# Kernel optimization log

Measured on AMD Instinct MI355X. Metric: run time of the kernel, lower is better.

## Reference

```python
import jax, jax.numpy as jnp
import numpy as np

N = 50000      # nodes
E = 800000     # edges
F_IN = 256
H1, D1 = 4, 32   # conv1 heads, per-head dim (hidden_features)
H2, D2 = 1, 32   # conv2 heads, per-head dim (out_features)
NEG_SLOPE = 0.2


def setup_inputs():
    key = jax.random.key(0)
    ks = jax.random.split(key, 12)
    x = jax.random.normal(ks[0], (N, F_IN), dtype=jnp.float32)
    src = jax.random.randint(ks[1], (E,), 0, N, dtype=jnp.int32)
    dst = jax.random.randint(ks[2], (E,), 0, N, dtype=jnp.int32)
    s = 0.05
    W1 = jax.random.normal(ks[3], (F_IN, H1 * D1), dtype=jnp.float32) * s
    al1 = jax.random.normal(ks[4], (H1, D1), dtype=jnp.float32) * s
    ar1 = jax.random.normal(ks[5], (H1, D1), dtype=jnp.float32) * s
    b1 = jnp.zeros((H1 * D1,), dtype=jnp.float32)
    W2 = jax.random.normal(ks[6], (H1 * D1, H2 * D2), dtype=jnp.float32) * s
    al2 = jax.random.normal(ks[7], (H2, D2), dtype=jnp.float32) * s
    ar2 = jax.random.normal(ks[8], (H2, D2), dtype=jnp.float32) * s
    b2 = jnp.zeros((H2 * D2,), dtype=jnp.float32)
    return {"x": x, "W1": W1, "al1": al1, "ar1": ar1, "b1": b1,
            "W2": W2, "al2": al2, "ar2": ar2, "b2": b2,
            "src": src, "dst": dst}


def gat_layer(x, W, al, ar, b, src, dst, H, D):
    # x: [N, F] -> feat: [N, H, D]
    feat = (x @ W).reshape(-1, H, D)
    el = jnp.sum(feat * al, axis=-1)   # [N, H]
    er = jnp.sum(feat * ar, axis=-1)   # [N, H]
    # per-edge attention logits, LeakyReLU
    e = jax.nn.leaky_relu(el[src] + er[dst], negative_slope=NEG_SLOPE)  # [E, H]
    # edge softmax over destination neighborhoods (stable)
    m = jax.ops.segment_max(e, dst, num_segments=N)          # [N, H]
    m = jnp.where(jnp.isfinite(m), m, 0.0)                   # guard zero-in-degree
    ee = jnp.exp(e - m[dst])                                 # [E, H]
    z = jax.ops.segment_sum(ee, dst, num_segments=N)         # [N, H]
    a = ee / jnp.maximum(z[dst], 1e-16)                      # [E, H]
    # weighted message aggregation
    msg = feat[src] * a[:, :, None]                          # [E, H, D]
    rst = jax.ops.segment_sum(msg, dst, num_segments=N)      # [N, H, D]
    return (rst + b.reshape(1, H, D)).reshape(-1, H * D)     # flatten(1)


def reference(x, W1, al1, ar1, b1, W2, al2, ar2, b2, src, dst):
    # dropouts are identity in eval mode; is_out_layer=True => no activation
    h = gat_layer(x, W1, al1, ar1, b1, src, dst, H1, D1)     # [N, H1*D1]
    out = gat_layer(h, W2, al2, ar2, b2, src, dst, H2, D2)   # [N, H2*D2]
    return out
```

## Files before the change

kernel.cpp:

```cpp
#include <hip/hip_runtime.h>

constexpr int F_IN = 256;
constexpr int H1 = 4, D1 = 32, F1 = H1 * D1;
constexpr int H2 = 1, D2 = 32, F2 = H2 * D2;
constexpr float NEG = 0.2f;

constexpr int BW = 128;
constexpr int NBUK_MAX = 512;
constexpr int CB = 128;

typedef short short8 __attribute__((ext_vector_type(8)));
typedef float f32x4 __attribute__((ext_vector_type(4)));

__device__ inline float bf2f(unsigned short u) {
    unsigned int x = ((unsigned int)u) << 16;
    return __builtin_bit_cast(float, x);
}
__device__ inline unsigned short f2bf(float f) {
    __bf16 h = (__bf16)f;
    return __builtin_bit_cast(unsigned short, h);
}

__global__ __launch_bounds__(256) void chist(const int* __restrict__ dst,
                                             unsigned int* __restrict__ HcT,
                                             int E, int nbuk) {
    __shared__ unsigned int h[NBUK_MAX];
    int tid = threadIdx.x;
    for (int i = tid; i < nbuk; i += 256) h[i] = 0;
    __syncthreads();
    int epb = (E + CB - 1) / CB;
    int e0 = blockIdx.x * epb, e1 = min(e0 + epb, E);
    for (int e = e0 + tid; e < e1; e += 256)
        atomicAdd(&h[dst[e] >> 7], 1u);
    __syncthreads();
    for (int i = tid; i < nbuk; i += 256) HcT[(size_t)i * CB + blockIdx.x] = h[i];
}

__global__ __launch_bounds__(512) void bscan(const unsigned int* __restrict__ HcT,
                                             unsigned int* __restrict__ Bb,
                                             unsigned int* __restrict__ S, int nbuk) {
    __shared__ unsigned int tot[NBUK_MAX];
    int t = threadIdx.x;
    unsigned int run = 0;
    if (t < nbuk) {
        const uint4* row = (const uint4*)(HcT + (size_t)t * CB);
#pragma unroll 8
        for (int b4 = 0; b4 < CB / 4; ++b4) {
            uint4 v = row[b4];
            int b = b4 * 4;
            Bb[(size_t)(b + 0) * nbuk + t] = run; run += v.x;
            Bb[(size_t)(b + 1) * nbuk + t] = run; run += v.y;
            Bb[(size_t)(b + 2) * nbuk + t] = run; run += v.z;
            Bb[(size_t)(b + 3) * nbuk + t] = run; run += v.w;
        }
    }
    tot[t] = (t < nbuk) ? run : 0;
    __syncthreads();
    for (int o = 1; o < NBUK_MAX; o <<= 1) {
        unsigned int v = (t >= o) ? tot[t - o] : 0;
        __syncthreads();
        tot[t] += v;
        __syncthreads();
    }
    if (t < nbuk) S[t] = tot[t] - run;
    if (t == nbuk - 1) S[nbuk] = tot[t];
}

__global__ __launch_bounds__(256) void cscat(const int* __restrict__ src,
                                             const int* __restrict__ dst,
                                             const unsigned int* __restrict__ Bb,
                                             const unsigned int* __restrict__ S,
                                             unsigned int* __restrict__ pairs, int E, int nbuk) {
    __shared__ unsigned int h[NBUK_MAX];
    int tid = threadIdx.x;
    for (int i = tid; i < nbuk; i += 256) h[i] = 0;
    __syncthreads();
    int epb = (E + CB - 1) / CB;
    int e0 = blockIdx.x * epb, e1 = min(e0 + epb, E);
    const unsigned int* bb = Bb + (size_t)blockIdx.x * nbuk;
    for (int e = e0 + tid; e < e1; e += 256) {
        int d = dst[e];
        int k = d >> 7;
        unsigned int r = atomicAdd(&h[k], 1u);
        unsigned int p = S[k] + bb[k] + r;
        pairs[p] = ((unsigned int)(d & 127) << 17) | (unsigned int)src[e];
    }
}

__global__ __launch_bounds__(256) void fscat(const unsigned int* __restrict__ pairs,
                                             const unsigned int* __restrict__ S,
                                             int* __restrict__ off, int* __restrict__ csr,
                                             int n, int E) {
    int k = blockIdx.x;
    int tid = threadIdx.x;
    unsigned int s0 = S[k], s1 = S[k + 1];
    __shared__ unsigned int cnt[BW];
    __shared__ unsigned int ex[BW];
    if (tid < BW) cnt[tid] = 0;
    __syncthreads();
    for (unsigned int i = s0 + tid; i < s1; i += 256)
        atomicAdd(&cnt[pairs[i] >> 17], 1u);
    __syncthreads();
    unsigned int orig = (tid < BW) ? cnt[tid] : 0;
    if (tid < BW) ex[tid] = orig;
    __syncthreads();
    for (int o = 1; o < BW; o <<= 1) {
        unsigned int v = (tid < BW && tid >= (unsigned)o) ? ex[tid - o] : 0;
        __syncthreads();
        if (tid < BW) ex[tid] += v;
        __syncthreads();
    }
    if (tid < BW) {
        ex[tid] -= orig;
        int node = k * BW + tid;
        if (node < n) off[node] = (int)(s0 + ex[tid]);
    }
    if (tid < BW) cnt[tid] = 0;
    __syncthreads();
    for (unsigned int i = s0 + tid; i < s1; i += 256) {
        unsigned int pr = pairs[i];
        int loc = pr >> 17;
        unsigned int r = atomicAdd(&cnt[loc], 1u);
        csr[s0 + ex[loc] + r] = (int)(pr & 0x1FFFFu);
    }
    if (k == 0 && tid == 0) off[n] = E;
}

__device__ inline void wsplit_one(const float* W, unsigned short* Wh, unsigned short* Wl,
                                  int idx, int C) {
    int j    = idx & 7;
    int lane = (idx >> 3) & 63;
    int t    = idx >> 9;
    int FC   = C >> 4;
    int fc   = t % FC, ks = t / FC;
    int k = ks * 32 + (lane >> 4) * 8 + j;
    int c = fc * 16 + (lane & 15);
    float v = W[(size_t)k * C + c];
    __bf16 h = (__bf16)v;
    float hv = (float)h;
    __bf16 lo = (__bf16)(v - hv);
    Wh[idx] = __builtin_bit_cast(unsigned short, h);
    Wl[idx] = __builtin_bit_cast(unsigned short, lo);
}
__global__ void wsplit_swz2(const float* __restrict__ W1, unsigned short* __restrict__ W1h,
                            unsigned short* __restrict__ W1l,
                            const float* __restrict__ W2, unsigned short* __restrict__ W2h,
                            unsigned short* __restrict__ W2l) {
    int idx = blockIdx.x * 256 + threadIdx.x;
    constexpr int N1 = F_IN * F1;
    if (idx < N1) wsplit_one(W1, W1h, W1l, idx, F1);
    else if (idx < N1 + F1 * F2) wsplit_one(W2, W2h, W2l, idx - N1, F2);
}

constexpr int BM1 = 64;
__global__ __launch_bounds__(256) void gemm1_mfma(
    const float* __restrict__ X,
    const unsigned short* __restrict__ Wh,
    const unsigned short* __restrict__ Wl,
    const float* __restrict__ alv, const float* __restrict__ arv,
    unsigned short* __restrict__ outb,
    float* __restrict__ el, float* __restrict__ er, int n)
{
    __shared__ float xs[64 * BM1 * 4];
    const int tid  = threadIdx.x;
    const int lane = tid & 63;
    const int wid  = tid >> 6;
    const int wrow = (wid >> 1) * 32;
    const int wcol = (wid & 1) * 64;
    const int wc16 = wcol >> 4;
    const int row0 = blockIdx.x * BM1;
    const int l16  = lane & 15;
    const int khi  = lane >> 4;

    {
        int gr = row0 + lane;
        gr = gr < n ? gr : (n - 1);
        const float* rowp = X + (size_t)gr * F_IN;
#pragma unroll
        for (int i = 0; i < 16; ++i) {
            int kc = wid * 16 + i;
            const float* srcp = rowp + kc * 4;
            float* dstf = &xs[kc * BM1 * 4];
            __builtin_amdgcn_global_load_lds(
                (const __attribute__((address_space(1))) unsigned int*)srcp,
                (__attribute__((address_space(3))) unsigned int*)dstf,
                16, 0, 0);
        }
    }
    asm volatile("s_waitcnt vmcnt(0)" ::: "memory");
    __syncthreads();

    f32x4 acc[2][4];
#pragma unroll
    for (int mi = 0; mi < 2; ++mi)
#pragma unroll
        for (int ni = 0; ni < 4; ++ni) acc[mi][ni] = f32x4{0.f, 0.f, 0.f, 0.f};

    short8 bh[2][4], bl[2][4];
#pragma unroll
    for (int ni = 0; ni < 4; ++ni) {
        int base = ((0 * 8 + wc16 + ni) * 64 + lane) * 8;
        bh[0][ni] = *(const short8*)(Wh + base);
        bl[0][ni] = *(const short8*)(Wl + base);
    }

#pragma unroll
    for (int ks = 0; ks < 8; ++ks) {
        const int cur = ks & 1, nxt = cur ^ 1;
        if (ks < 7) {
#pragma unroll
            for (int ni = 0; ni < 4; ++ni) {
                int base = (((ks + 1) * 8 + wc16 + ni) * 64 + lane) * 8;
                bh[nxt][ni] = *(const short8*)(Wh + base);
                bl[nxt][ni] = *(const short8*)(Wl + base);
            }
        }

        const int kc = ks * 8 + khi * 2;
        short8 ah[2], al8[2];
#pragma unroll
        for (int mi = 0; mi < 2; ++mi) {
            const int rt = wrow + mi * 16 + l16;
            float4 xa0 = *(const float4*)&xs[(kc + 0) * BM1 * 4 + rt * 4];
            float4 xa1 = *(const float4*)&xs[(kc + 1) * BM1 * 4 + rt * 4];
            float v[8] = {xa0.x, xa0.y, xa0.z, xa0.w, xa1.x, xa1.y, xa1.z, xa1.w};
#pragma unroll
            for (int j = 0; j < 8; ++j) {
                __bf16 h = (__bf16)v[j];
                float hv = (float)h;
                __bf16 lo = (__bf16)(v[j] - hv);
                ah[mi][j] = __builtin_bit_cast(short, h);
                al8[mi][j] = __builtin_bit_cast(short, lo);
            }
        }

#pragma unroll
        for (int mi = 0; mi < 2; ++mi)
#pragma unroll
            for (int ni = 0; ni < 4; ++ni) {
                acc[mi][ni] = __builtin_amdgcn_mfma_f32_16x16x32_bf16(al8[mi], bh[cur][ni], acc[mi][ni], 0, 0, 0);
                acc[mi][ni] = __builtin_amdgcn_mfma_f32_16x16x32_bf16(ah[mi], bl[cur][ni], acc[mi][ni], 0, 0, 0);
                acc[mi][ni] = __builtin_amdgcn_mfma_f32_16x16x32_bf16(ah[mi], bh[cur][ni], acc[mi][ni], 0, 0, 0);
            }
    }

    const int hh0 = wcol >> 5;
    float alr[2][2], arr[2][2];
#pragma unroll
    for (int t = 0; t < 2; ++t) {
        int head = hh0 + t;
        alr[t][0] = alv[head * 32 + l16];
        alr[t][1] = alv[head * 32 + 16 + l16];
        arr[t][0] = arv[head * 32 + l16];
        arr[t][1] = arv[head * 32 + 16 + l16];
    }

#pragma unroll
    for (int mi = 0; mi < 2; ++mi) {
        int rbase = row0 + wrow + mi * 16 + khi * 4;
#pragma unroll
        for (int rr = 0; rr < 4; ++rr) {
            int row = rbase + rr;
            bool ok = row < n;
            if (ok) {
#pragma unroll
                for (int ni = 0; ni < 4; ++ni)
                    outb[(size_t)row * F1 + wcol + ni * 16 + l16] = f2bf(acc[mi][ni][rr]);
            }
#pragma unroll
            for (int t = 0; t < 2; ++t) {
                float pel = acc[mi][2 * t][rr] * alr[t][0] + acc[mi][2 * t + 1][rr] * alr[t][1];
                float per = acc[mi][2 * t][rr] * arr[t][0] + acc[mi][2 * t + 1][rr] * arr[t][1];
#pragma unroll
                for (int o = 1; o < 16; o <<= 1) {
                    pel += __shfl_xor(pel, o);
                    per += __shfl_xor(per, o);
                }
                if (ok && l16 == 0) {
                    el[(size_t)row * H1 + hh0 + t] = pel;
                    er[(size_t)row * H1 + hh0 + t] = per;
                }
            }
        }
    }
}

constexpr int BM2 = 64;
__global__ __launch_bounds__(256) void gemm2_mfma(
    const float* __restrict__ X,
    const unsigned short* __restrict__ Wh,
    const unsigned short* __restrict__ Wl,
    const float* __restrict__ alv, const float* __restrict__ arv,
    float* __restrict__ out,
    float* __restrict__ el, float* __restrict__ er, int n)
{
    __shared__ float xs[32 * BM2 * 4];
    const int tid  = threadIdx.x;
    const int lane = tid & 63;
    const int wid  = tid >> 6;
    const int wrow = wid * 16;
    const int row0 = blockIdx.x * BM2;
    const int l16  = lane & 15;
    const int khi  = lane >> 4;

    {
        int gr = row0 + lane;
        gr = gr < n ? gr : (n - 1);
        const float* rowp = X + (size_t)gr * F1;
#pragma unroll
        for (int i = 0; i < 8; ++i) {
            int kc = wid * 8 + i;
            const float* srcp = rowp + kc * 4;
            float* dstf = &xs[kc * BM2 * 4];
            __builtin_amdgcn_global_load_lds(
                (const __attribute__((address_space(1))) unsigned int*)srcp,
                (__attribute__((address_space(3))) unsigned int*)dstf,
                16, 0, 0);
        }
    }
    asm volatile("s_waitcnt vmcnt(0)" ::: "memory");
    __syncthreads();

    f32x4 acc[2];
#pragma unroll
    for (int ni = 0; ni < 2; ++ni) acc[ni] = f32x4{0.f, 0.f, 0.f, 0.f};

    const int rt = wrow + l16;

#pragma unroll
    for (int ks = 0; ks < 4; ++ks) {
        const int kc = ks * 8 + khi * 2;

        short8 bh[2], bl[2];
#pragma unroll
        for (int ni = 0; ni < 2; ++ni) {
            int base = ((ks * 2 + ni) * 64 + lane) * 8;
            bh[ni] = *(const short8*)(Wh + base);
            bl[ni] = *(const short8*)(Wl + base);
        }

        float4 xa0 = *(const float4*)&xs[(kc + 0) * BM2 * 4 + rt * 4];
        float4 xa1 = *(const float4*)&xs[(kc + 1) * BM2 * 4 + rt * 4];
        float v[8] = {xa0.x, xa0.y, xa0.z, xa0.w, xa1.x, xa1.y, xa1.z, xa1.w};
        short8 ah, al8;
#pragma unroll
        for (int j = 0; j < 8; ++j) {
            __bf16 h = (__bf16)v[j];
            float hv = (float)h;
            __bf16 lo = (__bf16)(v[j] - hv);
            ah[j] = __builtin_bit_cast(short, h);
            al8[j] = __builtin_bit_cast(short, lo);
        }

#pragma unroll
        for (int ni = 0; ni < 2; ++ni) {
            acc[ni] = __builtin_amdgcn_mfma_f32_16x16x32_bf16(al8, bh[ni], acc[ni], 0, 0, 0);
            acc[ni] = __builtin_amdgcn_mfma_f32_16x16x32_bf16(ah, bl[ni], acc[ni], 0, 0, 0);
            acc[ni] = __builtin_amdgcn_mfma_f32_16x16x32_bf16(ah, bh[ni], acc[ni], 0, 0, 0);
        }
    }

    float al0 = alv[l16], al1c = alv[16 + l16];
    float ar0 = arv[l16], ar1c = arv[16 + l16];

    int rbase = row0 + wrow + khi * 4;
#pragma unroll
    for (int rr = 0; rr < 4; ++rr) {
        int row = rbase + rr;
        bool ok = row < n;
        if (ok) {
#pragma unroll
            for (int ni = 0; ni < 2; ++ni)
                out[(size_t)row * F2 + ni * 16 + l16] = acc[ni][rr];
        }
        float pel = acc[0][rr] * al0 + acc[1][rr] * al1c;
        float per = acc[0][rr] * ar0 + acc[1][rr] * ar1c;
#pragma unroll
        for (int o = 1; o < 16; o <<= 1) {
            pel += __shfl_xor(pel, o);
            per += __shfl_xor(per, o);
        }
        if (ok && l16 == 0) {
            el[row] = pel;
            er[row] = per;
        }
    }
}

__global__ __launch_bounds__(256) void agg1_kernel(
    const int* __restrict__ off, const int* __restrict__ csr_src,
    const unsigned short* __restrict__ featb, const float* __restrict__ el,
    const float* __restrict__ er, const float* __restrict__ b,
    float* __restrict__ out, int n)
{
    int wid = (blockIdx.x * 256 + threadIdx.x) >> 6;
    int lane = threadIdx.x & 63;
    if (wid >= n) return;
    int c0 = (lane & 31) * 4;
    int h = (lane & 31) >> 3;
    int half = lane >> 5;
    float erv = er[(size_t)wid * H1 + h];
    float sw = 0.f;
    float4 acc = {0.f, 0.f, 0.f, 0.f};
    int jb = off[wid], je = off[wid + 1];
    int j = jb + half;
    for (; j + 6 < je; j += 8) {
        int s0 = csr_src[j];
        int s1 = csr_src[j + 2];
        int s2 = csr_src[j + 4];
        int s3 = csr_src[j + 6];
        ushort4 u0 = *(const ushort4*)(featb + (size_t)s0 * F1 + c0);
        ushort4 u1 = *(const ushort4*)(featb + (size_t)s1 * F1 + c0);
        ushort4 u2 = *(const ushort4*)(featb + (size_t)s2 * F1 + c0);
        ushort4 u3 = *(const ushort4*)(featb + (size_t)s3 * F1 + c0);
        float t0 = el[(size_t)s0 * H1 + h] + erv;
        float t1 = el[(size_t)s1 * H1 + h] + erv;
        float t2 = el[(size_t)s2 * H1 + h] + erv;
        float t3 = el[(size_t)s3 * H1 + h] + erv;
        t0 = t0 > 0.f ? t0 : NEG * t0;
        t1 = t1 > 0.f ? t1 : NEG * t1;
        t2 = t2 > 0.f ? t2 : NEG * t2;
        t3 = t3 > 0.f ? t3 : NEG * t3;
        float w0 = __expf(t0), w1 = __expf(t1), w2 = __expf(t2), w3 = __expf(t3);
        sw += (w0 + w1) + (w2 + w3);
        acc.x = fmaf(w0, bf2f(u0.x), fmaf(w1, bf2f(u1.x), fmaf(w2, bf2f(u2.x), fmaf(w3, bf2f(u3.x), acc.x))));
        acc.y = fmaf(w0, bf2f(u0.y), fmaf(w1, bf2f(u1.y), fmaf(w2, bf2f(u2.y), fmaf(w3, bf2f(u3.y), acc.y))));
        acc.z = fmaf(w0, bf2f(u0.z), fmaf(w1, bf2f(u1.z), fmaf(w2, bf2f(u2.z), fmaf(w3, bf2f(u3.z), acc.z))));
        acc.w = fmaf(w0, bf2f(u0.w), fmaf(w1, bf2f(u1.w), fmaf(w2, bf2f(u2.w), fmaf(w3, bf2f(u3.w), acc.w))));
    }
    for (; j < je; j += 2) {
        int s = csr_src[j];
        ushort4 u = *(const ushort4*)(featb + (size_t)s * F1 + c0);
        float t = el[(size_t)s * H1 + h] + erv;
        t = t > 0.f ? t : NEG * t;
        float w = __expf(t);
        sw += w;
        acc.x = fmaf(w, bf2f(u.x), acc.x);
        acc.y = fmaf(w, bf2f(u.y), acc.y);
        acc.z = fmaf(w, bf2f(u.z), acc.z);
        acc.w = fmaf(w, bf2f(u.w), acc.w);
    }
    acc.x += __shfl_xor(acc.x, 32);
    acc.y += __shfl_xor(acc.y, 32);
    acc.z += __shfl_xor(acc.z, 32);
    acc.w += __shfl_xor(acc.w, 32);
    sw    += __shfl_xor(sw, 32);
    if (half == 0) {
        float inv = 1.f / fmaxf(sw, 1e-16f);
        float4 bb = *(const float4*)(b + c0);
        float4 t = {acc.x * inv + bb.x, acc.y * inv + bb.y,
                    acc.z * inv + bb.z, acc.w * inv + bb.w};
        *(float4*)(out + (size_t)wid * F1 + c0) = t;
    }
}

__global__ __launch_bounds__(256) void agg2_kernel(
    const int* __restrict__ off, const int* __restrict__ csr_src,
    const float* __restrict__ feat, const float* __restrict__ el,
    const float* __restrict__ er, const float* __restrict__ b,
    float* __restrict__ out, int n)
{
    int wid = (blockIdx.x * 256 + threadIdx.x) >> 6;
    int lane = threadIdx.x & 63;
    if (wid >= n) return;
    int c0 = (lane & 7) * 4;
    int grp = lane >> 3;
    float erv = er[wid];
    float sw = 0.f;
    float4 acc = {0.f, 0.f, 0.f, 0.f};
    int jb = off[wid], je = off[wid + 1];
    int j = jb + grp;
    for (; j + 8 < je; j += 16) {
        int s0 = csr_src[j];
        int s1 = csr_src[j + 8];
        float4 f0 = *(const float4*)(feat + (size_t)s0 * F2 + c0);
        float4 f1 = *(const float4*)(feat + (size_t)s1 * F2 + c0);
        float t0 = el[s0] + erv;
        float t1 = el[s1] + erv;
        t0 = t0 > 0.f ? t0 : NEG * t0;
        t1 = t1 > 0.f ? t1 : NEG * t1;
        float w0 = __expf(t0);
        float w1 = __expf(t1);
        sw += w0 + w1;
        acc.x = fmaf(w0, f0.x, fmaf(w1, f1.x, acc.x));
        acc.y = fmaf(w0, f0.y, fmaf(w1, f1.y, acc.y));
        acc.z = fmaf(w0, f0.z, fmaf(w1, f1.z, acc.z));
        acc.w = fmaf(w0, f0.w, fmaf(w1, f1.w, acc.w));
    }
    for (; j < je; j += 8) {
        int s = csr_src[j];
        float4 f = *(const float4*)(feat + (size_t)s * F2 + c0);
        float t = el[s] + erv;
        t = t > 0.f ? t : NEG * t;
        float w = __expf(t);
        sw += w;
        acc.x = fmaf(w, f.x, acc.x);
        acc.y = fmaf(w, f.y, acc.y);
        acc.z = fmaf(w, f.z, acc.z);
        acc.w = fmaf(w, f.w, acc.w);
    }
#pragma unroll
    for (int o = 8; o < 64; o <<= 1) {
        acc.x += __shfl_xor(acc.x, o);
        acc.y += __shfl_xor(acc.y, o);
        acc.z += __shfl_xor(acc.z, o);
        acc.w += __shfl_xor(acc.w, o);
        sw    += __shfl_xor(sw, o);
    }
    if (lane < 8) {
        float inv = 1.f / fmaxf(sw, 1e-16f);
        float4 bb = *(const float4*)(b + c0);
        float4 t = {acc.x * inv + bb.x, acc.y * inv + bb.y,
                    acc.z * inv + bb.z, acc.w * inv + bb.w};
        *(float4*)(out + (size_t)wid * F2 + c0) = t;
    }
}

extern "C" void kernel_launch(void* const* d_in, const int* in_sizes, int n_in,
                              void* d_out, int out_size, void* d_ws, size_t ws_size,
                              hipStream_t stream) {
    const float* x   = (const float*)d_in[0];
    const float* W1  = (const float*)d_in[1];
    const float* al1 = (const float*)d_in[2];
    const float* ar1 = (const float*)d_in[3];
    const float* b1  = (const float*)d_in[4];
    const float* W2  = (const float*)d_in[5];
    const float* al2 = (const float*)d_in[6];
    const float* ar2 = (const float*)d_in[7];
    const float* b2  = (const float*)d_in[8];
    const int*   src = (const int*)d_in[9];
    const int*   dst = (const int*)d_in[10];

    const int N = in_sizes[0] / F_IN;
    const int E = in_sizes[9];
    const int NBUK = (N + BW - 1) / BW;

    char* w = (char*)d_ws;
    size_t o = 0;
    auto alloc = [&](size_t bytes) { size_t cur = o; o += (bytes + 255) & ~255ULL; return cur; };
    int*   off   = (int*)  (w + alloc((size_t)(N + 1) * 4));
    int*   csr   = (int*)  (w + alloc((size_t)E * 4));
    unsigned int* pairs = (unsigned int*)(w + alloc((size_t)E * 4));
    unsigned int* HcT = (unsigned int*)(w + alloc((size_t)CB * NBUK * 4));
    unsigned int* Bb  = (unsigned int*)(w + alloc((size_t)CB * NBUK * 4));
    unsigned int* S   = (unsigned int*)(w + alloc((size_t)(NBUK + 1) * 4));
    unsigned short* feat1b = (unsigned short*)(w + alloc((size_t)N * F1 * 2));
    float* el1   = (float*)(w + alloc((size_t)N * H1 * 4));
    float* er1   = (float*)(w + alloc((size_t)N * H1 * 4));
    float* h1    = (float*)(w + alloc((size_t)N * F1 * 4));
    float* feat2 = (float*)(w + alloc((size_t)N * F2 * 4));
    float* el2   = (float*)(w + alloc((size_t)N * H2 * 4));
    float* er2   = (float*)(w + alloc((size_t)N * H2 * 4));
    unsigned short* W1h = (unsigned short*)(w + alloc((size_t)F_IN * F1 * 2));
    unsigned short* W1l = (unsigned short*)(w + alloc((size_t)F_IN * F1 * 2));
    unsigned short* W2h = (unsigned short*)(w + alloc((size_t)F1 * F2 * 2));
    unsigned short* W2l = (unsigned short*)(w + alloc((size_t)F1 * F2 * 2));
    (void)ws_size; (void)n_in; (void)out_size;

    chist<<<CB, 256, 0, stream>>>(dst, HcT, E, NBUK);
    bscan<<<1, 512, 0, stream>>>(HcT, Bb, S, NBUK);
    cscat<<<CB, 256, 0, stream>>>(src, dst, Bb, S, pairs, E, NBUK);
    fscat<<<NBUK, 256, 0, stream>>>(pairs, S, off, csr, N, E);

    wsplit_swz2<<<(F_IN * F1 + F1 * F2 + 255) / 256, 256, 0, stream>>>(
        W1, W1h, W1l, W2, W2h, W2l);

    gemm1_mfma<<<(N + BM1 - 1) / BM1, 256, 0, stream>>>(
        x, W1h, W1l, al1, ar1, feat1b, el1, er1, N);
    agg1_kernel<<<(N + 3) / 4, 256, 0, stream>>>(off, csr, feat1b, el1, er1, b1, h1, N);

    gemm2_mfma<<<(N + BM2 - 1) / BM2, 256, 0, stream>>>(
        h1, W2h, W2l, al2, ar2, feat2, el2, er2, N);
    agg2_kernel<<<(N + 3) / 4, 256, 0, stream>>>(off, csr, feat2, el2, er2, b2, (float*)d_out, N);
}
```

Measured before the change: 150.4 us.

## Pre-convert X to swizzled bf16 in a separate pass and drop its low-part product

Adds a kernel that converts x to bf16 and writes it in the MFMA fragment layout. gemm1 then loads A fragments straight from global memory, with no LDS staging and no per-iteration split. It also drops the x-low-part MFMA term, going from three bf16 MFMAs per tile to two, and removes the W register double buffering. This lowers precision on x, which may affect tolerance, and adds an extra full pass that reads x and writes a bf16 copy.

```diff
diff --git a/kernel.cpp b/kernel.cpp
--- a/kernel.cpp
+++ b/kernel.cpp
@@ -152,16 +152,46 @@
     else if (idx < N1 + F1 * F2) wsplit_one(W2, W2h, W2l, idx - N1, F2);
 }
 
+__global__ __launch_bounds__(256) void xswz_kernel(const float* __restrict__ x,
+                                                   unsigned short* __restrict__ xb,
+                                                   int n, int nrow_pad) {
+    int tid = threadIdx.x;
+    int lane = tid & 63;
+    int wid = tid >> 6;
+    int half = lane >> 5;
+    int l32 = lane & 31;
+    int ks = l32 >> 2;
+    int khi = l32 & 3;
+    int row = blockIdx.x * 8 + wid * 2 + half;
+    if (row >= nrow_pad) return;
+    float v[8];
+    if (row < n) {
+        const float* p = x + (size_t)row * F_IN + ks * 32 + khi * 8;
+        float4 a = *(const float4*)p;
+        float4 b = *(const float4*)(p + 4);
+        v[0] = a.x; v[1] = a.y; v[2] = a.z; v[3] = a.w;
+        v[4] = b.x; v[5] = b.y; v[6] = b.z; v[7] = b.w;
+    } else {
+#pragma unroll
+        for (int j = 0; j < 8; ++j) v[j] = 0.f;
+    }
+    short8 s;
+#pragma unroll
+    for (int j = 0; j < 8; ++j) s[j] = (short)f2bf(v[j]);
+    int frag16 = row >> 4;
+    int fragLane = (row & 15) | (khi << 4);
+    *(short8*)(xb + (((size_t)frag16 * 8 + ks) * 64 + fragLane) * 8) = s;
+}
+
 constexpr int BM1 = 64;
 __global__ __launch_bounds__(256) void gemm1_mfma(
-    const float* __restrict__ X,
+    const unsigned short* __restrict__ Xb,
     const unsigned short* __restrict__ Wh,
     const unsigned short* __restrict__ Wl,
     const float* __restrict__ alv, const float* __restrict__ arv,
     unsigned short* __restrict__ outb,
     float* __restrict__ el, float* __restrict__ er, int n)
 {
-    __shared__ float xs[64 * BM1 * 4];
     const int tid  = threadIdx.x;
     const int lane = tid & 63;
     const int wid  = tid >> 6;
@@ -171,24 +201,7 @@
     const int row0 = blockIdx.x * BM1;
     const int l16  = lane & 15;
     const int khi  = lane >> 4;
-
-    {
-        int gr = row0 + lane;
-        gr = gr < n ? gr : (n - 1);
-        const float* rowp = X + (size_t)gr * F_IN;
-#pragma unroll
-        for (int i = 0; i < 16; ++i) {
-            int kc = wid * 16 + i;
-            const float* srcp = rowp + kc * 4;
-            float* dstf = &xs[kc * BM1 * 4];
-            __builtin_amdgcn_global_load_lds(
-                (const __attribute__((address_space(1))) unsigned int*)srcp,
-                (__attribute__((address_space(3))) unsigned int*)dstf,
-                16, 0, 0);
-        }
-    }
-    asm volatile("s_waitcnt vmcnt(0)" ::: "memory");
-    __syncthreads();
+    const int fbase = blockIdx.x * 4 + (wid >> 1) * 2;
 
     f32x4 acc[2][4];
 #pragma unroll
@@ -196,51 +209,27 @@
 #pragma unroll
         for (int ni = 0; ni < 4; ++ni) acc[mi][ni] = f32x4{0.f, 0.f, 0.f, 0.f};
 
-    short8 bh[2][4], bl[2][4];
-#pragma unroll
-    for (int ni = 0; ni < 4; ++ni) {
-        int base = ((0 * 8 + wc16 + ni) * 64 + lane) * 8;
-        bh[0][ni] = *(const short8*)(Wh + base);
-        bl[0][ni] = *(const short8*)(Wl + base);
-    }
-
 #pragma unroll
     for (int ks = 0; ks < 8; ++ks) {
-        const int cur = ks & 1, nxt = cur ^ 1;
-        if (ks < 7) {
+        short8 ah[2];
+#pragma unroll
+        for (int mi = 0; mi < 2; ++mi)
+            ah[mi] = *(const short8*)(Xb + (((size_t)(fbase + mi) * 8 + ks) * 64 + lane) * 8);
+
+        short8 bh[4], bl[4];
+#pragma unroll
+        for (int ni = 0; ni < 4; ++ni) {
+            int base = ((ks * 8 + wc16 + ni) * 64 + lane) * 8;
+            bh[ni] = *(const short8*)(Wh + base);
+            bl[ni] = *(const short8*)(Wl + base);
+        }
+
+#pragma unroll
+        for (int mi = 0; mi < 2; ++mi)
 #pragma unroll
             for (int ni = 0; ni < 4; ++ni) {
-                int base = (((ks + 1) * 8 + wc16 + ni) * 64 + lane) * 8;
-                bh[nxt][ni] = *(const short8*)(Wh + base);
-                bl[nxt][ni] = *(const short8*)(Wl + base);
-            }
-        }
-
-        const int kc = ks * 8 + khi * 2;
-        short8 ah[2], al8[2];
-#pragma unroll
-        for (int mi = 0; mi < 2; ++mi) {
-            const int rt = wrow + mi * 16 + l16;
-            float4 xa0 = *(const float4*)&xs[(kc + 0) * BM1 * 4 + rt * 4];
-            float4 xa1 = *(const float4*)&xs[(kc + 1) * BM1 * 4 + rt * 4];
-            float v[8] = {xa0.x, xa0.y, xa0.z, xa0.w, xa1.x, xa1.y, xa1.z, xa1.w};
-#pragma unroll
-            for (int j = 0; j < 8; ++j) {
-                __bf16 h = (__bf16)v[j];
-                float hv = (float)h;
-                __bf16 lo = (__bf16)(v[j] - hv);
-                ah[mi][j] = __builtin_bit_cast(short, h);
-                al8[mi][j] = __builtin_bit_cast(short, lo);
-            }
-        }
-
-#pragma unroll
-        for (int mi = 0; mi < 2; ++mi)
-#pragma unroll
-            for (int ni = 0; ni < 4; ++ni) {
-                acc[mi][ni] = __builtin_amdgcn_mfma_f32_16x16x32_bf16(al8[mi], bh[cur][ni], acc[mi][ni], 0, 0, 0);
-                acc[mi][ni] = __builtin_amdgcn_mfma_f32_16x16x32_bf16(ah[mi], bl[cur][ni], acc[mi][ni], 0, 0, 0);
-                acc[mi][ni] = __builtin_amdgcn_mfma_f32_16x16x32_bf16(ah[mi], bh[cur][ni], acc[mi][ni], 0, 0, 0);
+                acc[mi][ni] = __builtin_amdgcn_mfma_f32_16x16x32_bf16(ah[mi], bl[ni], acc[mi][ni], 0, 0, 0);
+                acc[mi][ni] = __builtin_amdgcn_mfma_f32_16x16x32_bf16(ah[mi], bh[ni], acc[mi][ni], 0, 0, 0);
             }
     }
 
@@ -534,6 +523,8 @@
     const int N = in_sizes[0] / F_IN;
     const int E = in_sizes[9];
     const int NBUK = (N + BW - 1) / BW;
+    const int NBLK1 = (N + BM1 - 1) / BM1;
+    const int NROWP = NBLK1 * BM1;
 
     char* w = (char*)d_ws;
     size_t o = 0;
@@ -544,6 +535,7 @@
     unsigned int* HcT = (unsigned int*)(w + alloc((size_t)CB * NBUK * 4));
     unsigned int* Bb  = (unsigned int*)(w + alloc((size_t)CB * NBUK * 4));
     unsigned int* S   = (unsigned int*)(w + alloc((size_t)(NBUK + 1) * 4));
+    unsigned short* xb = (unsigned short*)(w + alloc((size_t)NROWP * F_IN * 2));
     unsigned short* feat1b = (unsigned short*)(w + alloc((size_t)N * F1 * 2));
     float* el1   = (float*)(w + alloc((size_t)N * H1 * 4));
     float* er1   = (float*)(w + alloc((size_t)N * H1 * 4));
@@ -564,9 +556,10 @@
 
     wsplit_swz2<<<(F_IN * F1 + F1 * F2 + 255) / 256, 256, 0, stream>>>(
         W1, W1h, W1l, W2, W2h, W2l);
-
-    gemm1_mfma<<<(N + BM1 - 1) / BM1, 256, 0, stream>>>(
-        x, W1h, W1l, al1, ar1, feat1b, el1, er1, N);
+    xswz_kernel<<<(NROWP + 7) / 8, 256, 0, stream>>>(x, xb, N, NROWP);
+
+    gemm1_mfma<<<NBLK1, 256, 0, stream>>>(
+        xb, W1h, W1l, al1, ar1, feat1b, el1, er1, N);
     agg1_kernel<<<(N + 3) / 4, 256, 0, stream>>>(off, csr, feat1b, el1, er1, b1, h1, N);
 
     gemm2_mfma<<<(N + BM2 - 1) / BM2, 256, 0, stream>>>(
```

Result: no change. 151.1 us (+0.5%).
